# Performance work log

Hardware: AMD Instinct MI355X
Metric: run time of the kernel (lower is better)

The kernel has to match this reference:

```python
import jax, jax.numpy as jnp
import numpy as np

B, S, H = 2, 2048, 2048
NH, NKV, HD = 16, 4, 128
ROPE_BASE = 10000.0


def rotate_half(x):
    x1, x2 = jnp.split(x, 2, axis=-1)
    return jnp.concatenate((-x2, x1), axis=-1)


def setup_inputs() -> dict:
    key = jax.random.key(0)
    ks = jax.random.split(key, 6)
    hidden_states = jax.random.normal(ks[0], (B, S, H), dtype=jnp.float32)
    # additive causal mask, as used by HF: 0 on allowed, large negative on masked
    causal = jnp.triu(jnp.full((S, S), -1e9, dtype=jnp.float32), k=1)
    attention_mask = jnp.broadcast_to(causal[None, None], (B, 1, S, S))
    position_ids = jnp.broadcast_to(jnp.arange(S, dtype=jnp.int64)[None], (B, S))
    scale = 1.0 / np.sqrt(H)
    Wq = jax.random.normal(ks[1], (NH * HD, H), dtype=jnp.float32) * scale
    Wk = jax.random.normal(ks[2], (NKV * HD, H), dtype=jnp.float32) * scale
    Wv = jax.random.normal(ks[3], (NKV * HD, H), dtype=jnp.float32) * scale
    Wo = jax.random.normal(ks[4], (H, NH * HD), dtype=jnp.float32) * scale
    return {"hidden_states": hidden_states, "attention_mask": attention_mask,
            "position_ids": position_ids, "Wq": Wq, "Wk": Wk, "Wv": Wv, "Wo": Wo}


def reference(hidden_states, attention_mask, position_ids, Wq, Wk, Wv, Wo):
    b, s, _ = hidden_states.shape
    # projections (torch Linear: y = x W^T)
    q = jnp.einsum('bsh,oh->bso', hidden_states, Wq).reshape(b, s, NH, HD).transpose(0, 2, 1, 3)
    k = jnp.einsum('bsh,oh->bso', hidden_states, Wk).reshape(b, s, NKV, HD).transpose(0, 2, 1, 3)
    v = jnp.einsum('bsh,oh->bso', hidden_states, Wv).reshape(b, s, NKV, HD).transpose(0, 2, 1, 3)
    # RoPE
    inv_freq = 1.0 / (ROPE_BASE ** (jnp.arange(0, HD, 2, dtype=jnp.float32) / HD))  # [HD/2]
    freqs = position_ids.astype(jnp.float32)[:, :, None] * inv_freq[None, None, :]  # [B,S,HD/2]
    emb = jnp.concatenate((freqs, freqs), axis=-1)                                  # [B,S,HD]
    cos = jnp.cos(emb)[:, None]  # [B,1,S,HD]
    sin = jnp.sin(emb)[:, None]
    q = q * cos + rotate_half(q) * sin
    k = k * cos + rotate_half(k) * sin
    # GQA repeat (repeat_interleave along head axis)
    n_rep = NH // NKV
    k = jnp.repeat(k, n_rep, axis=1)
    v = jnp.repeat(v, n_rep, axis=1)
    scale = HD ** -0.5
    attn = jnp.einsum('bhqd,bhkd->bhqk', q, k) * scale
    attn = attn + attention_mask
    attn = jax.nn.softmax(attn.astype(jnp.float32), axis=-1).astype(q.dtype)
    out = jnp.einsum('bhqk,bhkd->bhqd', attn, v)            # [B,NH,S,HD]
    out = out.transpose(0, 2, 1, 3).reshape(b, s, NH * HD)  # [B,S,H]
    return jnp.einsum('bso,ho->bsh', out, Wo)
```

## Files before the change

kernel.cpp:

```cpp
#include <hip/hip_runtime.h>


#define B_ 2
#define S_ 2048
#define H_ 2048
#define NH_ 16
#define NKV_ 4
#define HD_ 128
#define QKV_N 3072

typedef unsigned short u16;
typedef unsigned int u32;
typedef __attribute__((ext_vector_type(8))) short short8;
typedef __attribute__((ext_vector_type(4))) float floatx4;

__device__ __forceinline__ u16 f2bf(float f) {
    union { float f; u32 u; } v; v.f = f;
    u32 u = v.u;
    return (u16)((u + 0x7fffu + ((u >> 16) & 1u)) >> 16);
}
__device__ __forceinline__ float bf2f(u16 h) {
    union { u32 u; float f; } v; v.u = ((u32)h) << 16;
    return v.f;
}
__device__ __forceinline__ void store_out(u16* p, float v)  { *p = f2bf(v); }
__device__ __forceinline__ void store_out(float* p, float v) { *p = v; }

__device__ __forceinline__ void gload_lds16(const void* g, void* l) {
    __builtin_amdgcn_global_load_lds(
        (const __attribute__((address_space(1))) void*)g,
        (__attribute__((address_space(3))) void*)l, 16, 0, 0);
}

__global__ __launch_bounds__(256) void cast_f32_bf16(const float* __restrict__ in,
                                                     u16* __restrict__ out, int n) {
    int i = (blockIdx.x * 256 + threadIdx.x) * 4;
    if (i + 3 < n) {
        float4 f = *(const float4*)(in + i);
        out[i + 0] = f2bf(f.x);
        out[i + 1] = f2bf(f.y);
        out[i + 2] = f2bf(f.z);
        out[i + 3] = f2bf(f.w);
    }
}

template <typename OutT>
__global__ __launch_bounds__(256) void gemm128(const u16* __restrict__ A,
                                               const u16* __restrict__ Bm,
                                               OutT* __restrict__ C,
                                               int M, int N, int K) {
    __shared__ __align__(16) u16 As[128][32];
    __shared__ __align__(16) u16 Bs[128][32];
    const int tid  = threadIdx.x;
    const int wave = tid >> 6;
    const int lane = tid & 63;
    const int quad = lane >> 4;
    const int l16  = lane & 15;
    const int m0 = blockIdx.y * 128;
    const int n0 = blockIdx.x * 128;
    const int wm = (wave >> 1) * 64;
    const int wn = (wave & 1) * 64;
    const int srow = tid >> 2;
    const int scol = (tid & 3) * 8;

    floatx4 acc[4][4] = {};

    for (int k0 = 0; k0 < K; k0 += 32) {
        __syncthreads();
        gload_lds16(A  + (size_t)(m0 + srow) * K + k0 + scol,      &As[srow][scol]);
        gload_lds16(A  + (size_t)(m0 + 64 + srow) * K + k0 + scol, &As[64 + srow][scol]);
        gload_lds16(Bm + (size_t)(n0 + srow) * K + k0 + scol,      &Bs[srow][scol]);
        gload_lds16(Bm + (size_t)(n0 + 64 + srow) * K + k0 + scol, &Bs[64 + srow][scol]);
        __syncthreads();
        short8 af[4], bfv[4];
        for (int i = 0; i < 4; ++i) {
            af[i]  = *(const short8*)&As[wm + i * 16 + l16][quad * 8];
            bfv[i] = *(const short8*)&Bs[wn + i * 16 + l16][quad * 8];
        }
        for (int mi = 0; mi < 4; ++mi)
            for (int ni = 0; ni < 4; ++ni)
                acc[mi][ni] = __builtin_amdgcn_mfma_f32_16x16x32_bf16(
                    af[mi], bfv[ni], acc[mi][ni], 0, 0, 0);
    }
    for (int mi = 0; mi < 4; ++mi)
        for (int ni = 0; ni < 4; ++ni)
            for (int r = 0; r < 4; ++r) {
                int row = m0 + wm + mi * 16 + quad * 4 + r;
                int col = n0 + wn + ni * 16 + l16;
                store_out(C + (size_t)row * N + col, acc[mi][ni][r]);
            }
}

__global__ __launch_bounds__(256) void rope_kernel(u16* buf, int hofs, int nheads,
                                                   int total, float oscale) {
    int i = blockIdx.x * 256 + threadIdx.x;
    if (i >= total) return;
    int d = i & 63;
    int t = i >> 6;
    int head = t % nheads;
    int row  = t / nheads;
    int s    = row & (S_ - 1);
    size_t base = (size_t)row * QKV_N + hofs + head * HD_;
    float invf = exp2f(-(float)d * (13.28771237954945f / 64.0f));
    float fr = (float)s * invf;
    float sn, cs;
    sincosf(fr, &sn, &cs);
    float x1 = bf2f(buf[base + d]);
    float x2 = bf2f(buf[base + d + 64]);
    buf[base + d]      = f2bf((x1 * cs - x2 * sn) * oscale);
    buf[base + d + 64] = f2bf((x2 * cs + x1 * sn) * oscale);
}

__global__ __launch_bounds__(256) void transpose_v(const u16* __restrict__ qkv,
                                                   u16* __restrict__ vt) {
    __shared__ u16 t[32][33];
    const int tx = threadIdx.x, ty = threadIdx.y;
    const int c0 = blockIdx.x * 32, s0 = blockIdx.y * 32, b = blockIdx.z;
    for (int i = 0; i < 4; ++i)
        t[ty + i * 8][tx] =
            qkv[((size_t)(b * S_ + s0 + ty + i * 8)) * QKV_N + 2560 + c0 + tx];
    __syncthreads();
    for (int i = 0; i < 4; ++i)
        vt[((size_t)(b * 512 + c0 + ty + i * 8)) * S_ + s0 + tx] = t[tx][ty + i * 8];
}

__global__ __launch_bounds__(256, 4) void flash_attn(const u16* __restrict__ qkv,
                                                     const u16* __restrict__ vtg,
                                                     u16* __restrict__ o) {
    __shared__ __align__(16) u16 Ks[64][132];
    __shared__ __align__(16) u16 Vt[128][68];

    const int tid  = threadIdx.x;
    const int wave = tid >> 6;
    const int lane = tid & 63;
    const int quad = lane >> 4;
    const int l16  = lane & 15;

    const int bx = (int)blockIdx.x;
    const int by = (int)blockIdx.y;
    const int flip = (by >> 3) & 1;
    const int a4 = bx & 15;
    const int jq = flip ? a4 : (31 - a4);
    const int bh = (by & 7) | (((by >> 4) & 1) << 3) | ((bx >> 4) << 4);
    const int b   = bh >> 4;
    const int h   = bh & 15;
    const int kvh = h >> 2;
    const int q0  = jq * 64;

    const int qrow = q0 + wave * 16 + l16;
    const size_t qbase = ((size_t)(b * S_ + qrow)) * QKV_N + h * HD_;
    short8 qf[4];
#pragma unroll
    for (int ks = 0; ks < 4; ++ks)
        qf[ks] = *(const short8*)(qkv + qbase + ks * 32 + quad * 8);

    floatx4 o_acc[8] = {};
    float l_loc = 0.f;

    const int bsel = quad & 1;
    const int L0 = (bsel * 2) * 16 + l16;
    const int L1 = (bsel * 2 + 1) * 16 + l16;

    short8 kreg[4], vreg[4];
    int krow_[4], kc_[4], vd_[4], vc_[4];
#pragma unroll
    for (int p = 0; p < 4; ++p) {
        int idx  = p * 256 + tid;
        krow_[p] = idx >> 4;  kc_[p] = (idx & 15) * 8;
        vd_[p]   = idx >> 3;  vc_[p] = (idx & 7) * 8;
    }
    const size_t kbase = ((size_t)(b * S_)) * QKV_N + 2048 + kvh * HD_;
    const size_t vbase = ((size_t)((b * NKV_ + kvh) * HD_)) * S_;

#pragma unroll
    for (int p = 0; p < 4; ++p) {
        kreg[p] = *(const short8*)(qkv + kbase + (size_t)(krow_[p]) * QKV_N + kc_[p]);
        vreg[p] = *(const short8*)(vtg + vbase + (size_t)(vd_[p]) * S_ + vc_[p]);
    }

    for (int kt = 0; kt <= jq; ++kt) {
        __syncthreads();
#pragma unroll
        for (int p = 0; p < 4; ++p) {
            *(short8*)&Ks[krow_[p]][kc_[p]] = kreg[p];
            *(short8*)&Vt[vd_[p]][vc_[p]]   = vreg[p];
        }
        __syncthreads();

        if (kt < jq) {
            const size_t ko = kbase + (size_t)((kt + 1) * 64) * QKV_N;
            const size_t vo = vbase + (kt + 1) * 64;
#pragma unroll
            for (int p = 0; p < 4; ++p) {
                kreg[p] = *(const short8*)(qkv + ko + (size_t)(krow_[p]) * QKV_N + kc_[p]);
                vreg[p] = *(const short8*)(vtg + vo + (size_t)(vd_[p]) * S_ + vc_[p]);
            }
        }

        floatx4 sc[4];
#pragma unroll
        for (int ni = 0; ni < 4; ++ni) {
            floatx4 a = {};
#pragma unroll
            for (int ks = 0; ks < 4; ++ks) {
                short8 kf = *(const short8*)&Ks[ni * 16 + l16][ks * 32 + quad * 8];
                a = __builtin_amdgcn_mfma_f32_16x16x32_bf16(kf, qf[ks], a, 0, 0, 0);
            }
            sc[ni] = a;
        }
        if (kt == jq) {
            int qy = wave * 16 + l16;
#pragma unroll
            for (int ni = 0; ni < 4; ++ni)
#pragma unroll
                for (int r = 0; r < 4; ++r)
                    if (ni * 16 + quad * 4 + r > qy) sc[ni][r] = -INFINITY;
        }
        u32 pk[4][2];
#pragma unroll
        for (int ni = 0; ni < 4; ++ni) {
            float p0 = __expf(sc[ni][0]);
            float p1 = __expf(sc[ni][1]);
            float p2 = __expf(sc[ni][2]);
            float p3 = __expf(sc[ni][3]);
            l_loc += (p0 + p1) + (p2 + p3);
            pk[ni][0] = ((u32)f2bf(p1) << 16) | f2bf(p0);
            pk[ni][1] = ((u32)f2bf(p3) << 16) | f2bf(p2);
        }
#pragma unroll
        for (int ks = 0; ks < 2; ++ks) {
            int n0 = 2 * ks, n1 = 2 * ks + 1;
            u32 a0 = (u32)__shfl((int)pk[n0][0], L0);
            u32 a1 = (u32)__shfl((int)pk[n0][1], L0);
            u32 a2 = (u32)__shfl((int)pk[n0][0], L1);
            u32 a3 = (u32)__shfl((int)pk[n0][1], L1);
            u32 b0 = (u32)__shfl((int)pk[n1][0], L0);
            u32 b1 = (u32)__shfl((int)pk[n1][1], L0);
            u32 b2 = (u32)__shfl((int)pk[n1][0], L1);
            u32 b3 = (u32)__shfl((int)pk[n1][1], L1);
            union { u32 u[4]; short8 s; } pa;
            bool hi = (quad >> 1) != 0;
            pa.u[0] = hi ? b0 : a0;
            pa.u[1] = hi ? b1 : a1;
            pa.u[2] = hi ? b2 : a2;
            pa.u[3] = hi ? b3 : a3;
#pragma unroll
            for (int ds = 0; ds < 8; ++ds) {
                short8 vb = *(const short8*)&Vt[ds * 16 + l16][ks * 32 + quad * 8];
                o_acc[ds] = __builtin_amdgcn_mfma_f32_16x16x32_bf16(pa.s, vb, o_acc[ds], 0, 0, 0);
            }
        }
    }
    float lt = l_loc;
    lt += __shfl_xor(lt, 16, 64);
    lt += __shfl_xor(lt, 32, 64);
    float linv[4];
#pragma unroll
    for (int r = 0; r < 4; ++r)
        linv[r] = 1.0f / __shfl(lt, quad * 4 + r, 64);
#pragma unroll
    for (int ds = 0; ds < 8; ++ds)
#pragma unroll
        for (int r = 0; r < 4; ++r) {
            int row = q0 + wave * 16 + quad * 4 + r;
            size_t ob = ((size_t)(b * S_ + row)) * H_ + h * HD_ + ds * 16 + l16;
            o[ob] = f2bf(o_acc[ds][r] * linv[r]);
        }
}

extern "C" void kernel_launch(void* const* d_in, const int* in_sizes, int n_in,
                              void* d_out, int out_size, void* d_ws, size_t ws_size,
                              hipStream_t stream) {
    const float* hs = (const float*)d_in[0];
    const float* Wq = (const float*)d_in[3];
    const float* Wk = (const float*)d_in[4];
    const float* Wv = (const float*)d_in[5];
    const float* Wo = (const float*)d_in[6];

    char* ws = (char*)d_ws;
    const size_t MB = 1024 * 1024;
    u16* hs_b   = (u16*)(ws + 0);
    u16* wqkv_b = (u16*)(ws + 16 * MB);
    u16* vt_b   = (u16*)(ws + 16 * MB);
    u16* wo_b   = (u16*)(ws + 28 * MB);
    u16* qkv    = (u16*)(ws + 36 * MB);

    const int M = B_ * S_;

    cast_f32_bf16<<<8192, 256, 0, stream>>>(hs, hs_b, M * H_);
    cast_f32_bf16<<<4096, 256, 0, stream>>>(Wq, wqkv_b, H_ * H_);
    cast_f32_bf16<<<1024, 256, 0, stream>>>(Wk, wqkv_b + 2048 * 2048, 512 * H_);
    cast_f32_bf16<<<1024, 256, 0, stream>>>(Wv, wqkv_b + 2560 * 2048, 512 * H_);
    cast_f32_bf16<<<4096, 256, 0, stream>>>(Wo, wo_b, H_ * H_);

    gemm128<u16><<<dim3(QKV_N / 128, M / 128), 256, 0, stream>>>(
        hs_b, wqkv_b, qkv, M, QKV_N, H_);

    rope_kernel<<<(M * NH_ * 64) / 256, 256, 0, stream>>>(
        qkv, 0, NH_, M * NH_ * 64, 0.08838834764831845f);
    rope_kernel<<<(M * NKV_ * 64) / 256, 256, 0, stream>>>(
        qkv, 2048, NKV_, M * NKV_ * 64, 1.0f);

    transpose_v<<<dim3(16, 64, 2), dim3(32, 8), 0, stream>>>(qkv, vt_b);

    flash_attn<<<dim3(32, 32), 256, 0, stream>>>(qkv, vt_b, hs_b);

    gemm128<float><<<dim3(H_ / 128, M / 128), 256, 0, stream>>>(
        hs_b, wo_b, (float*)d_out, M, H_, H_);
}
```

Measured before the change: 364.8 us.

## Rewrite flash attention with 32x32 MFMA, direct-to-LDS swizzled loads, split-K waves

Rewrites the attention kernel so each wave computes a 32x32 score tile with 32x32x16 bf16 MFMA, and pairs of waves split the key block and reduce partial outputs through LDS at the end. K and V tiles are loaded straight into LDS with global_load_lds and an XOR swizzle, which drops the register prefetch double-buffering. Probability packing now uses v_cvt_pk_bf16_f32 and permlane32_swap in place of shuffles, and the output store is vectorised. The cost is an extra cross-wave reduction with several barriers, and global-to-LDS loads that are no longer overlapped with compute.

Result: faster. 345.3 us (-5.4%).

```diff
diff --git a/kernel.cpp b/kernel.cpp
--- a/kernel.cpp
+++ b/kernel.cpp
@@ -11,8 +11,10 @@
 
 typedef unsigned short u16;
 typedef unsigned int u32;
+typedef unsigned long long u64;
 typedef __attribute__((ext_vector_type(8))) short short8;
 typedef __attribute__((ext_vector_type(4))) float floatx4;
+typedef __attribute__((ext_vector_type(16))) float floatx16;
 
 __device__ __forceinline__ u16 f2bf(float f) {
     union { float f; u32 u; } v; v.f = f;
@@ -30,6 +32,23 @@
     __builtin_amdgcn_global_load_lds(
         (const __attribute__((address_space(1))) void*)g,
         (__attribute__((address_space(3))) void*)l, 16, 0, 0);
+}
+
+__device__ __forceinline__ u32 cvtpk(float lo, float hi) {
+    u32 r;
+    asm("v_cvt_pk_bf16_f32 %0, %1, %2" : "=v"(r) : "v"(lo), "v"(hi));
+    return r;
+}
+
+__device__ __forceinline__ void pl32swap(u32& a, u32& b) {
+#if __has_builtin(__builtin_amdgcn_permlane32_swap)
+    typedef __attribute__((ext_vector_type(2))) int iv2;
+    iv2 r = __builtin_amdgcn_permlane32_swap((int)a, (int)b, false, false);
+    a = (u32)r[0];
+    b = (u32)r[1];
+#else
+    asm volatile("v_permlane32_swap_b32 %0, %1" : "+v"(a), "+v"(b));
+#endif
 }
 
 __global__ __launch_bounds__(256) void cast_f32_bf16(const float* __restrict__ in,
@@ -124,17 +143,19 @@
         vt[((size_t)(b * 512 + c0 + ty + i * 8)) * S_ + s0 + tx] = t[tx][ty + i * 8];
 }
 
-__global__ __launch_bounds__(256, 4) void flash_attn(const u16* __restrict__ qkv,
-                                                     const u16* __restrict__ vtg,
-                                                     u16* __restrict__ o) {
-    __shared__ __align__(16) u16 Ks[64][132];
-    __shared__ __align__(16) u16 Vt[128][68];
+__global__ __launch_bounds__(256) void flash_attn(const u16* __restrict__ qkv,
+                                                  const u16* __restrict__ vtg,
+                                                  u16* __restrict__ o) {
+    __shared__ __align__(16) u16 KsL[64 * 128];
+    __shared__ __align__(16) u16 VtL[128 * 64];
 
     const int tid  = threadIdx.x;
     const int wave = tid >> 6;
     const int lane = tid & 63;
-    const int quad = lane >> 4;
-    const int l16  = lane & 15;
+    const int l31  = lane & 31;
+    const int hi   = lane >> 5;
+    const int wq   = wave >> 1;
+    const int kb   = wave & 1;
 
     const int bx = (int)blockIdx.x;
     const int by = (int)blockIdx.y;
@@ -147,125 +168,115 @@
     const int kvh = h >> 2;
     const int q0  = jq * 64;
 
-    const int qrow = q0 + wave * 16 + l16;
-    const size_t qbase = ((size_t)(b * S_ + qrow)) * QKV_N + h * HD_;
-    short8 qf[4];
-#pragma unroll
-    for (int ks = 0; ks < 4; ++ks)
-        qf[ks] = *(const short8*)(qkv + qbase + ks * 32 + quad * 8);
-
-    floatx4 o_acc[8] = {};
+    const size_t qb = ((size_t)(b * S_ + q0 + wq * 32 + l31)) * QKV_N + h * HD_;
+    short8 qf[8];
+#pragma unroll
+    for (int mf = 0; mf < 8; ++mf)
+        qf[mf] = *(const short8*)(qkv + qb + mf * 16 + hi * 8);
+
+    floatx16 o_acc[4] = {};
     float l_loc = 0.f;
 
-    const int bsel = quad & 1;
-    const int L0 = (bsel * 2) * 16 + l16;
-    const int L1 = (bsel * 2 + 1) * 16 + l16;
-
-    short8 kreg[4], vreg[4];
-    int krow_[4], kc_[4], vd_[4], vc_[4];
-#pragma unroll
-    for (int p = 0; p < 4; ++p) {
-        int idx  = p * 256 + tid;
-        krow_[p] = idx >> 4;  kc_[p] = (idx & 15) * 8;
-        vd_[p]   = idx >> 3;  vc_[p] = (idx & 7) * 8;
+    const size_t kbase = (size_t)(b * S_) * QKV_N + 2048 + kvh * HD_;
+    const size_t vbase = (size_t)((b * NKV_ + kvh) * HD_) * S_;
+    const int krow_l = (lane >> 4);
+    const int kslot  = lane & 15;
+    const int vrow_l = (lane >> 3);
+    const int vslot  = lane & 7;
+
+    const int rk = kb * 32 + l31;
+    const int kswz = rk & 7;
+
+    for (int kt = 0; kt <= jq; ++kt) {
+        __syncthreads();
+#pragma unroll
+        for (int p = 0; p < 4; ++p) {
+            int r = 16 * wave + 4 * p + krow_l;
+            gload_lds16(qkv + kbase + (size_t)(kt * 64 + r) * QKV_N
+                            + ((kslot ^ (r & 7)) * 8),
+                        &KsL[(16 * wave + 4 * p) * 128 + lane * 8]);
+            int rv = 32 * wave + 8 * p + vrow_l;
+            gload_lds16(vtg + vbase + (size_t)rv * S_ + kt * 64
+                            + ((vslot ^ (rv & 7)) * 8),
+                        &VtL[(32 * wave + 8 * p) * 64 + lane * 8]);
+        }
+        __syncthreads();
+
+        floatx16 st = {};
+#pragma unroll
+        for (int mf = 0; mf < 8; ++mf) {
+            short8 kf = *(const short8*)&KsL[rk * 128 + (((mf * 2 + hi) ^ kswz) * 8)];
+            st = __builtin_amdgcn_mfma_f32_32x32x16_bf16(kf, qf[mf], st, 0, 0, 0);
+        }
+        if (kt == jq) {
+            int qloc = wq * 32 + l31;
+#pragma unroll
+            for (int r = 0; r < 16; ++r) {
+                int krow = kb * 32 + (r & 3) + 8 * (r >> 2) + 4 * hi;
+                if (krow > qloc) st[r] = -INFINITY;
+            }
+        }
+        u32 pk[8];
+        float ll = 0.f;
+#pragma unroll
+        for (int i = 0; i < 8; ++i) {
+            float e0 = __expf(st[2 * i]);
+            float e1 = __expf(st[2 * i + 1]);
+            ll += e0 + e1;
+            pk[i] = cvtpk(e0, e1);
+        }
+        l_loc += ll;
+        pl32swap(pk[0], pk[2]);
+        pl32swap(pk[1], pk[3]);
+        pl32swap(pk[4], pk[6]);
+        pl32swap(pk[5], pk[7]);
+        union { u32 u[4]; short8 s; } c0, c1;
+        c0.u[0] = pk[0]; c0.u[1] = pk[1]; c0.u[2] = pk[2]; c0.u[3] = pk[3];
+        c1.u[0] = pk[4]; c1.u[1] = pk[5]; c1.u[2] = pk[6]; c1.u[3] = pk[7];
+#pragma unroll
+        for (int dblk = 0; dblk < 4; ++dblk) {
+            int rv = dblk * 32 + l31;
+            int sw = rv & 7;
+            short8 va = *(const short8*)&VtL[rv * 64 + (((kb * 4 + hi) ^ sw) * 8)];
+            o_acc[dblk] = __builtin_amdgcn_mfma_f32_32x32x16_bf16(va, c0.s, o_acc[dblk], 0, 0, 0);
+            short8 vb = *(const short8*)&VtL[rv * 64 + (((kb * 4 + 2 + hi) ^ sw) * 8)];
+            o_acc[dblk] = __builtin_amdgcn_mfma_f32_32x32x16_bf16(vb, c1.s, o_acc[dblk], 0, 0, 0);
+        }
     }
-    const size_t kbase = ((size_t)(b * S_)) * QKV_N + 2048 + kvh * HD_;
-    const size_t vbase = ((size_t)((b * NKV_ + kvh) * HD_)) * S_;
-
-#pragma unroll
-    for (int p = 0; p < 4; ++p) {
-        kreg[p] = *(const short8*)(qkv + kbase + (size_t)(krow_[p]) * QKV_N + kc_[p]);
-        vreg[p] = *(const short8*)(vtg + vbase + (size_t)(vd_[p]) * S_ + vc_[p]);
+
+    float lt = l_loc + __shfl_xor(l_loc, 32, 64);
+    __syncthreads();
+    float* scr = (float*)KsL;
+    if (kb == 1) scr[wq * 64 + lane] = lt;
+    __syncthreads();
+    float linv = 0.f;
+    if (kb == 0) linv = 1.0f / (lt + scr[wq * 64 + lane]);
+
+#pragma unroll
+    for (int dblk = 0; dblk < 4; ++dblk) {
+        __syncthreads();
+        if (kb == 1) {
+#pragma unroll
+            for (int r = 0; r < 16; ++r)
+                scr[wq * 1088 + lane * 17 + r] = o_acc[dblk][r];
+        }
+        __syncthreads();
+        if (kb == 0) {
+            const int row = q0 + wq * 32 + l31;
+#pragma unroll
+            for (int rg = 0; rg < 4; ++rg) {
+                float v0 = (o_acc[dblk][rg * 4 + 0] + scr[wq * 1088 + lane * 17 + rg * 4 + 0]) * linv;
+                float v1 = (o_acc[dblk][rg * 4 + 1] + scr[wq * 1088 + lane * 17 + rg * 4 + 1]) * linv;
+                float v2 = (o_acc[dblk][rg * 4 + 2] + scr[wq * 1088 + lane * 17 + rg * 4 + 2]) * linv;
+                float v3 = (o_acc[dblk][rg * 4 + 3] + scr[wq * 1088 + lane * 17 + rg * 4 + 3]) * linv;
+                u32 wlo = cvtpk(v0, v1);
+                u32 whi = cvtpk(v2, v3);
+                int col = h * HD_ + dblk * 32 + rg * 8 + 4 * hi;
+                u64 pack = (u64)wlo | ((u64)whi << 32);
+                *(u64*)(o + ((size_t)(b * S_ + row)) * H_ + col) = pack;
+            }
+        }
     }
-
-    for (int kt = 0; kt <= jq; ++kt) {
-        __syncthreads();
-#pragma unroll
-        for (int p = 0; p < 4; ++p) {
-            *(short8*)&Ks[krow_[p]][kc_[p]] = kreg[p];
-            *(short8*)&Vt[vd_[p]][vc_[p]]   = vreg[p];
-        }
-        __syncthreads();
-
-        if (kt < jq) {
-            const size_t ko = kbase + (size_t)((kt + 1) * 64) * QKV_N;
-            const size_t vo = vbase + (kt + 1) * 64;
-#pragma unroll
-            for (int p = 0; p < 4; ++p) {
-                kreg[p] = *(const short8*)(qkv + ko + (size_t)(krow_[p]) * QKV_N + kc_[p]);
-                vreg[p] = *(const short8*)(vtg + vo + (size_t)(vd_[p]) * S_ + vc_[p]);
-            }
-        }
-
-        floatx4 sc[4];
-#pragma unroll
-        for (int ni = 0; ni < 4; ++ni) {
-            floatx4 a = {};
-#pragma unroll
-            for (int ks = 0; ks < 4; ++ks) {
-                short8 kf = *(const short8*)&Ks[ni * 16 + l16][ks * 32 + quad * 8];
-                a = __builtin_amdgcn_mfma_f32_16x16x32_bf16(kf, qf[ks], a, 0, 0, 0);
-            }
-            sc[ni] = a;
-        }
-        if (kt == jq) {
-            int qy = wave * 16 + l16;
-#pragma unroll
-            for (int ni = 0; ni < 4; ++ni)
-#pragma unroll
-                for (int r = 0; r < 4; ++r)
-                    if (ni * 16 + quad * 4 + r > qy) sc[ni][r] = -INFINITY;
-        }
-        u32 pk[4][2];
-#pragma unroll
-        for (int ni = 0; ni < 4; ++ni) {
-            float p0 = __expf(sc[ni][0]);
-            float p1 = __expf(sc[ni][1]);
-            float p2 = __expf(sc[ni][2]);
-            float p3 = __expf(sc[ni][3]);
-            l_loc += (p0 + p1) + (p2 + p3);
-            pk[ni][0] = ((u32)f2bf(p1) << 16) | f2bf(p0);
-            pk[ni][1] = ((u32)f2bf(p3) << 16) | f2bf(p2);
-        }
-#pragma unroll
-        for (int ks = 0; ks < 2; ++ks) {
-            int n0 = 2 * ks, n1 = 2 * ks + 1;
-            u32 a0 = (u32)__shfl((int)pk[n0][0], L0);
-            u32 a1 = (u32)__shfl((int)pk[n0][1], L0);
-            u32 a2 = (u32)__shfl((int)pk[n0][0], L1);
-            u32 a3 = (u32)__shfl((int)pk[n0][1], L1);
-            u32 b0 = (u32)__shfl((int)pk[n1][0], L0);
-            u32 b1 = (u32)__shfl((int)pk[n1][1], L0);
-            u32 b2 = (u32)__shfl((int)pk[n1][0], L1);
-            u32 b3 = (u32)__shfl((int)pk[n1][1], L1);
-            union { u32 u[4]; short8 s; } pa;
-            bool hi = (quad >> 1) != 0;
-            pa.u[0] = hi ? b0 : a0;
-            pa.u[1] = hi ? b1 : a1;
-            pa.u[2] = hi ? b2 : a2;
-            pa.u[3] = hi ? b3 : a3;
-#pragma unroll
-            for (int ds = 0; ds < 8; ++ds) {
-                short8 vb = *(const short8*)&Vt[ds * 16 + l16][ks * 32 + quad * 8];
-                o_acc[ds] = __builtin_amdgcn_mfma_f32_16x16x32_bf16(pa.s, vb, o_acc[ds], 0, 0, 0);
-            }
-        }
-    }
-    float lt = l_loc;
-    lt += __shfl_xor(lt, 16, 64);
-    lt += __shfl_xor(lt, 32, 64);
-    float linv[4];
-#pragma unroll
-    for (int r = 0; r < 4; ++r)
-        linv[r] = 1.0f / __shfl(lt, quad * 4 + r, 64);
-#pragma unroll
-    for (int ds = 0; ds < 8; ++ds)
-#pragma unroll
-        for (int r = 0; r < 4; ++r) {
-            int row = q0 + wave * 16 + quad * 4 + r;
-            size_t ob = ((size_t)(b * S_ + row)) * H_ + h * HD_ + ds * 16 + l16;
-            o[ob] = f2bf(o_acc[ds][r] * linv[r]);
-        }
 }
 
 extern "C" void kernel_launch(void* const* d_in, const int* in_sizes, int n_in,
```
